# Kernel optimization log

Hardware: AMD Instinct MI355X
Metric: run time of the kernel (lower is better)

## Reference

```python
import jax, jax.numpy as jnp
import numpy as np

D_MODEL = 128; D_STATE = 64; HEADDIM = 64; CHUNK = 64; EXPAND = 2
D_INNER = EXPAND * D_MODEL            # 256
NHEADS = D_INNER // HEADDIM           # 4
NGROUPS = 1; D_CONV = 4
D_XBC = D_INNER + 2 * NGROUPS * D_STATE          # 384
D_IN_PROJ = 2 * D_INNER + 2 * NGROUPS * D_STATE + NHEADS  # 644


def _segsum(x):
    # x: (..., L) -> (..., L, L) with [i, j] = sum_{j<k<=i} x_k, -inf above diag
    L = x.shape[-1]
    cs = jnp.cumsum(x, -1)
    d = cs[..., :, None] - cs[..., None, :]
    mask = jnp.tril(jnp.ones((L, L), bool))
    return jnp.where(mask, d, -jnp.inf)


def _mamba2(x, Wi, conv_w, conv_b, dt_bias, A_log, Dp, norm_w, Wo):
    b, l, _ = x.shape
    zxbcdt = x @ Wi.T                                    # (b,l,644)
    z = zxbcdt[..., :D_INNER]
    xBC = zxbcdt[..., D_INNER:D_INNER + D_XBC]
    dt = jax.nn.softplus(zxbcdt[..., D_INNER + D_XBC:] + dt_bias)  # (b,l,h)
    # causal depthwise conv1d, kernel 4
    xp = jnp.pad(xBC, ((0, 0), (D_CONV - 1, 0), (0, 0)))
    xBC = sum(xp[:, k:k + l, :] * conv_w[:, k] for k in range(D_CONV)) + conv_b
    xBC = jax.nn.silu(xBC)
    xs = xBC[..., :D_INNER].reshape(b, l, NHEADS, HEADDIM)
    Bm = xBC[..., D_INNER:D_INNER + D_STATE]             # (b,l,n) ngroups=1
    Cm = xBC[..., D_INNER + D_STATE:]                    # (b,l,n)
    A = -jnp.exp(A_log)                                  # (h,)
    # chunked SSD (ssd_minimal style)
    c = l // CHUNK
    X = xs.reshape(b, c, CHUNK, NHEADS, HEADDIM)
    dtc = dt.reshape(b, c, CHUNK, NHEADS)
    Bc = Bm.reshape(b, c, CHUNK, D_STATE)
    Cc = Cm.reshape(b, c, CHUNK, D_STATE)
    dA = jnp.transpose(dtc * A, (0, 3, 1, 2))            # (b,h,c,L)
    Acs = jnp.cumsum(dA, -1)
    Lm = jnp.exp(_segsum(dA))                            # (b,h,c,L,L)
    Xdt = X * dtc[..., None]                             # (b,c,L,h,p)
    Yd = jnp.einsum('bcln,bcsn,bhcls,bcshp->bclhp', Cc, Bc, Lm, Xdt)
    dec = jnp.exp(Acs[..., -1:] - Acs)                   # (b,h,c,L)
    st = jnp.einsum('bcln,bhcl,bclhp->bchpn', Bc, dec, Xdt)  # per-chunk states
    cd = jnp.exp(Acs[..., -1])                           # (b,h,c)
    def step(carry, inp):
        s, d = inp                                       # s:(b,h,p,n), d:(b,h)
        return carry * d[..., None, None] + s, carry
    init = jnp.zeros_like(st[:, 0])
    _, prev = jax.lax.scan(step, init, (jnp.moveaxis(st, 1, 0), jnp.moveaxis(cd, 2, 0)))
    prev = jnp.moveaxis(prev, 0, 1)                      # (b,c,h,p,n)
    Yo = jnp.einsum('bcln,bchpn,bhcl->bclhp', Cc, prev, jnp.exp(Acs))
    Y = (Yd + Yo).reshape(b, l, NHEADS, HEADDIM) + Dp[None, None, :, None] * xs
    # gated RMSNorm (norm_before_gate=False)
    y = Y.reshape(b, l, D_INNER) * jax.nn.silu(z)
    y = y * jax.lax.rsqrt(jnp.mean(y * y, -1, keepdims=True) + 1e-5) * norm_w
    return y @ Wo.T


def _init_params(key):
    ks = jax.random.split(key, 5)
    dt = jnp.exp(jax.random.uniform(ks[2], (NHEADS,)) * (np.log(0.1) - np.log(0.001)) + np.log(0.001))
    return {
        'Wi': jax.random.normal(ks[0], (D_IN_PROJ, D_MODEL), jnp.float32) * (D_MODEL ** -0.5),
        'conv_w': jax.random.normal(ks[1], (D_XBC, D_CONV), jnp.float32) * 0.3,
        'conv_b': jnp.zeros((D_XBC,), jnp.float32),
        'dt_bias': jnp.log(jnp.expm1(dt)),
        'A_log': jnp.log(jax.random.uniform(ks[3], (NHEADS,)) * 15.0 + 1.0),
        'D': jnp.ones((NHEADS,), jnp.float32),
        'norm_w': jnp.ones((D_INNER,), jnp.float32),
        'Wo': jax.random.normal(ks[4], (D_MODEL, D_INNER), jnp.float32) * (D_INNER ** -0.5),
    }


def setup_inputs() -> dict:
    key = jax.random.key(0)
    kx, kf, kb = jax.random.split(key, 3)
    inp = {'x': jax.random.normal(kx, (16, 2048, D_MODEL), jnp.float32)}
    for sfx, kk in (('_f', kf), ('_b', kb)):
        p = _init_params(kk)
        for name, v in p.items():
            inp[name + sfx] = v
    return inp


def reference(x, Wi_f, conv_w_f, conv_b_f, dt_bias_f, A_log_f, D_f, norm_w_f, Wo_f,
              Wi_b, conv_w_b, conv_b_b, dt_bias_b, A_log_b, D_b, norm_w_b, Wo_b):
    h_f = _mamba2(x, Wi_f, conv_w_f, conv_b_f, dt_bias_f, A_log_f, D_f, norm_w_f, Wo_f)
    h_b = jnp.flip(_mamba2(jnp.flip(x, 1), Wi_b, conv_w_b, conv_b_b, dt_bias_b, A_log_b, D_b, norm_w_b, Wo_b), 1)
    return h_f + h_b
```

## Files before the change

### kernel.cpp

```cpp
#include <hip/hip_runtime.h>
#include <hip/hip_bf16.h>
#include <cmath>

#define B_    16
#define L_    2048
#define T_    32768
#define DM_   128
#define DI_   256
#define DXBC_ 384
#define DS_   64
#define HD_   64
#define NH_   4
#define NC_   32

typedef __hip_bfloat16 bf16;
typedef __attribute__((ext_vector_type(8))) short short8;
typedef __attribute__((ext_vector_type(4))) float f32x4;

__device__ __forceinline__ float b2f(bf16 v) { return __bfloat162float(v); }
__device__ __forceinline__ bf16  f2b(float f) { return __float2bfloat16(f); }
__device__ __forceinline__ short f2bs(float f) { bf16 h = __float2bfloat16(f); return *reinterpret_cast<short*>(&h); }
__device__ __forceinline__ float bs2f(short s) { bf16 h = *reinterpret_cast<bf16*>(&s); return __bfloat162float(h); }
__device__ __forceinline__ float sigmoidf_(float x) { return 1.f / (1.f + expf(-x)); }
__device__ __forceinline__ float softplusf_(float x) { return (x > 20.f) ? x : log1pf(expf(x)); }
__device__ __forceinline__ float expneg_(float x) { return expf(fminf(x, 0.f)); }

struct __align__(8) S4 { short a, b, c, d; };

#define NWI 82432
#define NWO 32768

__global__ __launch_bounds__(256) void k_prep(
    const float* __restrict__ x,
    const float* __restrict__ WiF, const float* __restrict__ WiB,
    const float* __restrict__ WoF, const float* __restrict__ WoB,
    bf16* __restrict__ Xb, bf16* __restrict__ WiFb, bf16* __restrict__ WiBb,
    bf16* __restrict__ WoFb, bf16* __restrict__ WoBb)
{
    const int gid = blockIdx.x * 256 + threadIdx.x;
    const int stride = gridDim.x * 256;
    for (int i = gid; i < 1048576; i += stride) {
        float4 v = ((const float4*)x)[i];
        S4 s = { f2bs(v.x), f2bs(v.y), f2bs(v.z), f2bs(v.w) };
        ((S4*)Xb)[i] = s;
    }
    for (int i = gid; i < NWI / 4; i += stride) {
        float4 v = ((const float4*)WiF)[i];
        S4 s = { f2bs(v.x), f2bs(v.y), f2bs(v.z), f2bs(v.w) };
        ((S4*)WiFb)[i] = s;
        v = ((const float4*)WiB)[i];
        S4 t = { f2bs(v.x), f2bs(v.y), f2bs(v.z), f2bs(v.w) };
        ((S4*)WiBb)[i] = t;
    }
    for (int i = gid; i < NWO / 4; i += stride) {
        float4 v = ((const float4*)WoF)[i];
        S4 s = { f2bs(v.x), f2bs(v.y), f2bs(v.z), f2bs(v.w) };
        ((S4*)WoFb)[i] = s;
        v = ((const float4*)WoB)[i];
        S4 t = { f2bs(v.x), f2bs(v.y), f2bs(v.z), f2bs(v.w) };
        ((S4*)WoBb)[i] = t;
    }
}

__global__ __launch_bounds__(256) void k_inproj_mfma(
    const bf16* __restrict__ Xb, const bf16* __restrict__ WiFb, const bf16* __restrict__ WiBb,
    const float* __restrict__ cwF, const float* __restrict__ cbF,
    const float* __restrict__ cwB, const float* __restrict__ cbB,
    const float* __restrict__ dtbF, const float* __restrict__ dtbB,
    bf16* __restrict__ Z, bf16* __restrict__ XBC, float* __restrict__ DTV)
{
    const int tid  = threadIdx.x;
    const int wave = tid >> 6, lane = tid & 63;
    const int ln15 = lane & 15, q = lane >> 4;
    const int dir  = blockIdx.y;
    const bf16* Wi = dir ? WiBb : WiFb;
    const int t0 = blockIdx.x * 64;
    const int batch = t0 >> 11, l0 = t0 & (L_ - 1);
    const size_t rowbase = (size_t)dir * T_ + t0;

    __shared__ __align__(16) short xs[80][136];
    __shared__ __align__(16) short smem2[64 * 136];
    short (*ws)[136]  = (short(*)[136])smem2;
    short (*raws)[72] = (short(*)[72])smem2;

    for (int u = tid; u < 1280; u += 256) {
        int r = u >> 4, g = u & 15;
        int l = l0 - 16 + r;
        short8 v = {0, 0, 0, 0, 0, 0, 0, 0};
        if (l >= 0) {
            int sl = dir ? (L_ - 1 - l) : l;
            v = *(const short8*)(Xb + ((size_t)batch * L_ + sl) * DM_ + g * 8);
        }
        *(short8*)&xs[r][g * 8] = v;
    }
    __syncthreads();

    for (int nt = 0; nt <= 10; ++nt) {
        const int c0 = nt * 64;
        __syncthreads();
        if (nt < 10) {
            for (int u = tid; u < 1024; u += 256) {
                int r = u >> 4, g = u & 15;
                *(short8*)&ws[r][g * 8] = *(const short8*)(Wi + (size_t)(c0 + r) * DM_ + g * 8);
            }
        } else {
            for (int u = tid; u < 1024; u += 256) {
                int r = u >> 4, g = u & 15;
                short8 v = {0, 0, 0, 0, 0, 0, 0, 0};
                if (r < 4) v = *(const short8*)(Wi + (size_t)(640 + r) * DM_ + g * 8);
                *(short8*)&ws[r][g * 8] = v;
            }
        }
        __syncthreads();

        f32x4 acc[5];
#pragma unroll
        for (int mt = 0; mt < 5; ++mt) acc[mt] = (f32x4){0.f, 0.f, 0.f, 0.f};
#pragma unroll
        for (int ks = 0; ks < 4; ++ks) {
            short8 bfr = *(const short8*)&ws[16 * wave + ln15][ks * 32 + q * 8];
#pragma unroll
            for (int mt = 0; mt < 5; ++mt) {
                short8 afr = *(const short8*)&xs[16 * mt + ln15][ks * 32 + q * 8];
                acc[mt] = __builtin_amdgcn_mfma_f32_16x16x32_bf16(afr, bfr, acc[mt], 0, 0, 0);
            }
        }

        if (nt == 10) {
            if (wave == 0 && ln15 < 4) {
                const float* dtb = dir ? dtbB : dtbF;
                float bias = dtb[ln15];
#pragma unroll
                for (int mt = 1; mt < 5; ++mt)
#pragma unroll
                    for (int rg = 0; rg < 4; ++rg) {
                        int row = 16 * (mt - 1) + 4 * q + rg;
                        DTV[(rowbase + row) * NH_ + ln15] = softplusf_(acc[mt][rg] + bias);
                    }
            }
            break;
        }

        __syncthreads();
#pragma unroll
        for (int mt = 0; mt < 5; ++mt)
#pragma unroll
            for (int rg = 0; rg < 4; ++rg)
                raws[16 * mt + 4 * q + rg][16 * wave + ln15] = f2bs(acc[mt][rg]);
        __syncthreads();

        if (nt < 4) {
            for (int u = tid; u < 1024; u += 256) {
                int row = u >> 4, c4 = (u & 15) * 4;
                S4 s = *(const S4*)&raws[16 + row][c4];
                *(S4*)(Z + (rowbase + row) * DI_ + c0 + c4) = s;
            }
        } else {
            const float* cw = dir ? cwB : cwF;
            const float* cb = dir ? cbB : cbF;
            for (int u = tid; u < 1024; u += 256) {
                int row = u >> 4, c4 = (u & 15) * 4;
                short o[4];
#pragma unroll
                for (int j = 0; j < 4; ++j) {
                    int ch = c0 - 256 + c4 + j;
                    float s = cb[ch];
#pragma unroll
                    for (int k = 0; k < 4; ++k) s += bs2f(raws[13 + row + k][c4 + j]) * cw[ch * 4 + k];
                    s = s * sigmoidf_(s);
                    o[j] = f2bs(s);
                }
                S4 s4 = { o[0], o[1], o[2], o[3] };
                *(S4*)(XBC + (rowbase + row) * DXBC_ + c0 - 256 + c4) = s4;
            }
        }
    }
}

__global__ __launch_bounds__(256) void k_chunkdiag_mfma(
    const bf16* __restrict__ XBC, const float* __restrict__ DTV,
    const float* __restrict__ AlF, const float* __restrict__ AlB,
    const float* __restrict__ DpF, const float* __restrict__ DpB,
    bf16* __restrict__ Y, bf16* __restrict__ ST, float* __restrict__ CDb)
{
    const int tid = threadIdx.x;
    const int wave = tid >> 6, lane = tid & 63;
    const int ln15 = lane & 15, q = lane >> 4;
    const int c = blockIdx.x;
    const int b = blockIdx.y >> 2;
    const int h = blockIdx.y & 3;
    const int dir = blockIdx.z;
    const float Ah = -expf((dir ? AlB : AlF)[h]);
    const float Dh = (dir ? DpB : DpF)[h];
    const int t0 = b * L_ + c * 64;
    const size_t rowbase = (size_t)dir * T_ + t0;

    __shared__ __align__(16) short Bs[64][72];
    __shared__ __align__(16) short Cs[64][72];
    __shared__ __align__(16) short Xt[64][72];
    __shared__ __align__(16) short Bt[64][72];
    __shared__ float dts[64];
    __shared__ float Acs[64];
    __shared__ float decs[64];

    if (tid < 64) {
        int l = tid;
        float dt = DTV[(rowbase + l) * NH_ + h];
        dts[l] = dt;
        float s = dt * Ah;
#pragma unroll
        for (int off = 1; off < 64; off <<= 1) {
            float t2 = __shfl_up(s, off);
            if (l >= off) s += t2;
        }
        Acs[l] = s;
        float alast = __shfl(s, 63);
        decs[l] = expneg_(alast - s);
        if (l == 0) CDb[(((size_t)dir * B_ + b) * NH_ + h) * NC_ + c] = expneg_(alast);
    }
    __syncthreads();

    for (int u = tid; u < 512; u += 256) {
        int r = u >> 3, g = u & 7;
        size_t base = (rowbase + r) * DXBC_;
        *(short8*)&Bs[r][g * 8] = *(const short8*)(XBC + base + 256 + g * 8);
        *(short8*)&Cs[r][g * 8] = *(const short8*)(XBC + base + 320 + g * 8);
    }
    for (int u = tid; u < 4096; u += 256) {
        int l = u >> 6, p = u & 63;
        Xt[p][l] = f2bs(b2f(XBC[(rowbase + l) * DXBC_ + h * HD_ + p]) * dts[l]);
    }
    for (int u = tid; u < 4096; u += 256) {
        int l = u >> 6, n = u & 63;
        Bt[n][l] = f2bs(b2f(XBC[(rowbase + l) * DXBC_ + 256 + n]) * decs[l]);
    }
    __syncthreads();

    f32x4 a1[4];
#pragma unroll
    for (int ct = 0; ct < 4; ++ct) a1[ct] = (f32x4){0.f, 0.f, 0.f, 0.f};
#pragma unroll
    for (int ks = 0; ks < 2; ++ks) {
        short8 afr = *(const short8*)&Cs[16 * wave + ln15][ks * 32 + q * 8];
#pragma unroll
        for (int ct = 0; ct < 4; ++ct) {
            short8 bfr = *(const short8*)&Bs[16 * ct + ln15][ks * 32 + q * 8];
            a1[ct] = __builtin_amdgcn_mfma_f32_16x16x32_bf16(afr, bfr, a1[ct], 0, 0, 0);
        }
    }
#pragma unroll
    for (int ct = 0; ct < 4; ++ct)
#pragma unroll
        for (int rg = 0; rg < 4; ++rg) {
            int l = 16 * wave + 4 * q + rg, s = 16 * ct + ln15;
            float m = (s <= l) ? a1[ct][rg] * expneg_(Acs[l] - Acs[s]) : 0.f;
            Cs[l][s] = f2bs(m);
        }
    f32x4 a2[4];
#pragma unroll
    for (int ct = 0; ct < 4; ++ct) a2[ct] = (f32x4){0.f, 0.f, 0.f, 0.f};
#pragma unroll
    for (int ks = 0; ks < 2; ++ks) {
        short8 afr = *(const short8*)&Cs[16 * wave + ln15][ks * 32 + q * 8];
#pragma unroll
        for (int ct = 0; ct < 4; ++ct) {
            short8 bfr = *(const short8*)&Xt[16 * ct + ln15][ks * 32 + q * 8];
            a2[ct] = __builtin_amdgcn_mfma_f32_16x16x32_bf16(afr, bfr, a2[ct], 0, 0, 0);
        }
    }
#pragma unroll
    for (int ct = 0; ct < 4; ++ct)
#pragma unroll
        for (int rg = 0; rg < 4; ++rg) {
            int l = 16 * wave + 4 * q + rg, p = 16 * ct + ln15;
            size_t tI = rowbase + l;
            float xraw = b2f(XBC[tI * DXBC_ + h * HD_ + p]);
            Y[tI * DI_ + h * HD_ + p] = f2b(a2[ct][rg] + Dh * xraw);
        }
    f32x4 a3[4];
#pragma unroll
    for (int ct = 0; ct < 4; ++ct) a3[ct] = (f32x4){0.f, 0.f, 0.f, 0.f};
#pragma unroll
    for (int ks = 0; ks < 2; ++ks) {
        short8 afr = *(const short8*)&Xt[16 * wave + ln15][ks * 32 + q * 8];
#pragma unroll
        for (int ct = 0; ct < 4; ++ct) {
            short8 bfr = *(const short8*)&Bt[16 * ct + ln15][ks * 32 + q * 8];
            a3[ct] = __builtin_amdgcn_mfma_f32_16x16x32_bf16(afr, bfr, a3[ct], 0, 0, 0);
        }
    }
    size_t sb = ((((size_t)dir * B_ + b) * NC_ + c) * NH_ + h) * 4096;
#pragma unroll
    for (int ct = 0; ct < 4; ++ct)
#pragma unroll
        for (int rg = 0; rg < 4; ++rg) {
            int p = 16 * wave + 4 * q + rg, n = 16 * ct + ln15;
            ST[sb + p * 64 + n] = f2b(a3[ct][rg]);
        }
}

__global__ __launch_bounds__(256) void k_scan(bf16* __restrict__ ST, const float* __restrict__ CDb)
{
    const int tid = threadIdx.x;
    const int dir = blockIdx.y;
    const int bx = blockIdx.x;
    const int b = bx >> 4, h = (bx >> 2) & 3, qt = bx & 3;
    const size_t cdbase = (((size_t)dir * B_ + b) * NH_ + h) * NC_;
    float carry[4] = {0.f, 0.f, 0.f, 0.f};
    for (int c = 0; c < NC_; ++c) {
        const float cd = CDb[cdbase + c];
        size_t base = ((((size_t)dir * B_ + b) * NC_ + c) * NH_ + h) * 4096 + qt * 1024 + tid;
#pragma unroll
        for (int q = 0; q < 4; ++q) {
            float v = b2f(ST[base + q * 256]);
            ST[base + q * 256] = f2b(carry[q]);
            carry[q] = carry[q] * cd + v;
        }
    }
}

__global__ __launch_bounds__(256) void k_offdiag_fused(
    const bf16* __restrict__ XBC, const float* __restrict__ DTV,
    const float* __restrict__ AlF, const float* __restrict__ AlB,
    const bf16* __restrict__ ST, const bf16* __restrict__ Z,
    const float* __restrict__ nwF, const float* __restrict__ nwB,
    bf16* __restrict__ Y)
{
    const int tid = threadIdx.x;
    const int wave = tid >> 6, lane = tid & 63;
    const int ln15 = lane & 15, q = lane >> 4;
    const int c = blockIdx.x, b = blockIdx.y, dir = blockIdx.z;
    const float* Al = dir ? AlB : AlF;
    const int t0 = b * L_ + c * 64;
    const size_t rowbase = (size_t)dir * T_ + t0;

    __shared__ __align__(16) short Cs[64][72];
    __shared__ __align__(16) short Ps[64][72];
    __shared__ __align__(16) short Yz[64][264];
    __shared__ float eA[NH_][64];

    {
        float A = -expf(Al[wave]);
        float s = DTV[(rowbase + lane) * NH_ + wave] * A;
#pragma unroll
        for (int off = 1; off < 64; off <<= 1) {
            float t2 = __shfl_up(s, off);
            if (lane >= off) s += t2;
        }
        eA[wave][lane] = expneg_(s);
    }
    for (int u = tid; u < 512; u += 256) {
        int r = u >> 3, g = u & 7;
        *(short8*)&Cs[r][g * 8] = *(const short8*)(XBC + (rowbase + r) * DXBC_ + 320 + g * 8);
    }
    for (int u = lane; u < 512; u += 64) {
        int r = 16 * wave + (u >> 5), g = u & 31;
        *(short8*)&Yz[r][g * 8] = *(const short8*)(Y + (rowbase + r) * DI_ + g * 8);
    }

    for (int h = 0; h < NH_; ++h) {
        __syncthreads();
        size_t sb = ((((size_t)dir * B_ + b) * NC_ + c) * NH_ + h) * 4096;
        for (int u = tid; u < 512; u += 256) {
            int r = u >> 3, g = u & 7;
            *(short8*)&Ps[r][g * 8] = *(const short8*)(ST + sb + r * 64 + g * 8);
        }
        __syncthreads();

        f32x4 acc[4];
#pragma unroll
        for (int ct = 0; ct < 4; ++ct) acc[ct] = (f32x4){0.f, 0.f, 0.f, 0.f};
#pragma unroll
        for (int ks = 0; ks < 2; ++ks) {
            short8 afr = *(const short8*)&Cs[16 * wave + ln15][ks * 32 + q * 8];
#pragma unroll
            for (int ct = 0; ct < 4; ++ct) {
                short8 bfr = *(const short8*)&Ps[16 * ct + ln15][ks * 32 + q * 8];
                acc[ct] = __builtin_amdgcn_mfma_f32_16x16x32_bf16(afr, bfr, acc[ct], 0, 0, 0);
            }
        }
#pragma unroll
        for (int ct = 0; ct < 4; ++ct)
#pragma unroll
            for (int rg = 0; rg < 4; ++rg) {
                int l = 16 * wave + 4 * q + rg, p = 16 * ct + ln15;
                float yv = bs2f(Yz[l][h * 64 + p]) + acc[ct][rg] * eA[h][l];
                Yz[l][h * 64 + p] = f2bs(yv);
            }
    }

    const float* nw = dir ? nwB : nwF;
    float nwv[4];
#pragma unroll
    for (int j = 0; j < 4; ++j) nwv[j] = nw[lane * 4 + j];
    for (int rr = 0; rr < 16; ++rr) {
        int row = 16 * wave + rr;
        S4 zv4 = *(const S4*)(Z + (rowbase + row) * DI_ + lane * 4);
        short zr[4] = { zv4.a, zv4.b, zv4.c, zv4.d };
        float v[4]; float ss = 0.f;
#pragma unroll
        for (int j = 0; j < 4; ++j) {
            float yv = bs2f(Yz[row][lane * 4 + j]);
            float zf = bs2f(zr[j]);
            v[j] = yv * zf * sigmoidf_(zf);
            ss += v[j] * v[j];
        }
#pragma unroll
        for (int off = 1; off < 64; off <<= 1) ss += __shfl_xor(ss, off);
        float rn = rsqrtf(ss * (1.f / 256.f) + 1e-5f);
        S4 o = { f2bs(v[0] * rn * nwv[0]), f2bs(v[1] * rn * nwv[1]),
                 f2bs(v[2] * rn * nwv[2]), f2bs(v[3] * rn * nwv[3]) };
        *(S4*)(Y + (rowbase + row) * DI_ + lane * 4) = o;
    }
}

__global__ __launch_bounds__(512) void k_outproj_mfma(
    const bf16* __restrict__ Y, const bf16* __restrict__ WoFb, const bf16* __restrict__ WoBb,
    float* __restrict__ out)
{
    const int tid = threadIdx.x;
    const int wave = tid >> 6, lane = tid & 63;
    const int ln15 = lane & 15, q = lane >> 4;
    const int mt = wave & 3, nh = wave >> 2;
    const int t0 = blockIdx.x * 64;
    const int batch = t0 >> 11;
    const int l0 = t0 & (L_ - 1);

    __shared__ __align__(16) short ys[64][72];
    __shared__ __align__(16) short wsm[128][72];

    f32x4 acc[4];
#pragma unroll
    for (int ct = 0; ct < 4; ++ct) acc[ct] = (f32x4){0.f, 0.f, 0.f, 0.f};

    for (int dir = 0; dir < 2; ++dir) {
        const bf16* Wo = dir ? WoBb : WoFb;
        for (int kt = 0; kt < 4; ++kt) {
            const int k0 = kt * 64;
            __syncthreads();
            {
                int u = tid;
                int r = u >> 3, g = u & 7;
                int tsrc = dir ? (batch * L_ + (L_ - 1 - (l0 + r))) : (t0 + r);
                *(short8*)&ys[r][g * 8] =
                    *(const short8*)(Y + ((size_t)dir * T_ + tsrc) * DI_ + k0 + g * 8);
            }
            for (int u = tid; u < 1024; u += 512) {
                int m = u >> 3, g = u & 7;
                *(short8*)&wsm[m][g * 8] = *(const short8*)(Wo + (size_t)m * DI_ + k0 + g * 8);
            }
            __syncthreads();
#pragma unroll
            for (int ks = 0; ks < 2; ++ks) {
                short8 afr = *(const short8*)&ys[16 * mt + ln15][ks * 32 + q * 8];
#pragma unroll
                for (int ct = 0; ct < 4; ++ct) {
                    short8 bfr = *(const short8*)&wsm[16 * (4 * nh + ct) + ln15][ks * 32 + q * 8];
                    acc[ct] = __builtin_amdgcn_mfma_f32_16x16x32_bf16(afr, bfr, acc[ct], 0, 0, 0);
                }
            }
        }
    }
#pragma unroll
    for (int ct = 0; ct < 4; ++ct)
#pragma unroll
        for (int rg = 0; rg < 4; ++rg) {
            int row = 16 * mt + 4 * q + rg, col = 16 * (4 * nh + ct) + ln15;
            out[((size_t)(t0 + row)) * DM_ + col] = acc[ct][rg];
        }
}

extern "C" void kernel_launch(void* const* d_in, const int* in_sizes, int n_in,
                              void* d_out, int out_size, void* d_ws, size_t ws_size,
                              hipStream_t stream)
{
    const float* x    = (const float*)d_in[0];
    const float* WiF  = (const float*)d_in[1];
    const float* cwF  = (const float*)d_in[2];
    const float* cbF  = (const float*)d_in[3];
    const float* dtbF = (const float*)d_in[4];
    const float* AlF  = (const float*)d_in[5];
    const float* DpF  = (const float*)d_in[6];
    const float* nwF  = (const float*)d_in[7];
    const float* WoF  = (const float*)d_in[8];
    const float* WiB  = (const float*)d_in[9];
    const float* cwB  = (const float*)d_in[10];
    const float* cbB  = (const float*)d_in[11];
    const float* dtbB = (const float*)d_in[12];
    const float* AlB  = (const float*)d_in[13];
    const float* DpB  = (const float*)d_in[14];
    const float* nwB  = (const float*)d_in[15];
    const float* WoB  = (const float*)d_in[16];

    const size_t nZ   = (size_t)2 * T_ * DI_;
    const size_t nXBC = (size_t)2 * T_ * DXBC_;
    const size_t nY   = (size_t)2 * T_ * DI_;
    const size_t nST  = (size_t)2 * B_ * NC_ * NH_ * HD_ * DS_;
    const size_t nWb  = (size_t)2 * NWI + 2 * NWO;
    const size_t nDTV = (size_t)2 * T_ * NH_;
    const size_t nCD  = (size_t)2 * B_ * NH_ * NC_;
    const size_t need = (nZ + nXBC + nY + nST + nWb) * sizeof(bf16)
                      + (nDTV + nCD) * sizeof(float);
    if (ws_size < need) return;

    char* p = (char*)d_ws;
    bf16* Z    = (bf16*)p;            p += nZ * sizeof(bf16);
    bf16* XBC  = (bf16*)p;            p += nXBC * sizeof(bf16);
    bf16* Yb   = (bf16*)p;            p += nY * sizeof(bf16);
    bf16* ST   = (bf16*)p;            p += nST * sizeof(bf16);
    bf16* WiFb = (bf16*)p;            p += (size_t)NWI * sizeof(bf16);
    bf16* WiBb = (bf16*)p;            p += (size_t)NWI * sizeof(bf16);
    bf16* WoFb = (bf16*)p;            p += (size_t)NWO * sizeof(bf16);
    bf16* WoBb = (bf16*)p;            p += (size_t)NWO * sizeof(bf16);
    float* DTV = (float*)p;           p += nDTV * sizeof(float);
    float* CDb = (float*)p;
    bf16* Xb   = ST;

    k_prep<<<2048, 256, 0, stream>>>(x, WiF, WiB, WoF, WoB, Xb, WiFb, WiBb, WoFb, WoBb);
    k_inproj_mfma<<<dim3(512, 2), 256, 0, stream>>>(Xb, WiFb, WiBb, cwF, cbF, cwB, cbB,
                                                    dtbF, dtbB, Z, XBC, DTV);
    k_chunkdiag_mfma<<<dim3(NC_, B_ * NH_, 2), 256, 0, stream>>>(XBC, DTV, AlF, AlB, DpF, DpB,
                                                                 Yb, ST, CDb);
    k_scan<<<dim3(256, 2), 256, 0, stream>>>(ST, CDb);
    k_offdiag_fused<<<dim3(NC_, B_, 2), 256, 0, stream>>>(XBC, DTV, AlF, AlB, ST, Z,
                                                          nwF, nwB, Yb);
    k_outproj_mfma<<<dim3(512), 512, 0, stream>>>(Yb, WoFb, WoBb, (float*)d_out);
}
```

Baseline: 285.6 us.

## Load projection weights directly into registers and restructure in/out projection kernels

The in-projection kernel now reads weight fragments straight from global memory into registers instead of staging them through shared memory. It also splits the Z tiles (written directly from accumulators with swapped MFMA operands), the conv tiles and the dt computation into separate loops, which removes several block barriers. The out-projection kernel drops to 256 threads, stages the full 256-wide Y row once per direction and reads Wo fragments directly from global/L2, so each wave computes all 128 output columns. This is meant to cut LDS traffic and synchronisation, at the cost of more uncoalesced global weight reads and more accumulator registers.

```diff
diff --git a/kernel.cpp b/kernel.cpp
--- a/kernel.cpp
+++ b/kernel.cpp
@@ -79,9 +79,7 @@
     const size_t rowbase = (size_t)dir * T_ + t0;
 
     __shared__ __align__(16) short xs[80][136];
-    __shared__ __align__(16) short smem2[64 * 136];
-    short (*ws)[136]  = (short(*)[136])smem2;
-    short (*raws)[72] = (short(*)[72])smem2;
+    __shared__ __align__(16) short raws[80][80];
 
     for (int u = tid; u < 1280; u += 256) {
         int r = u >> 4, g = u & 15;
@@ -95,52 +93,42 @@
     }
     __syncthreads();
 
-    for (int nt = 0; nt <= 10; ++nt) {
+#pragma unroll
+    for (int zt = 0; zt < 4; ++zt) {
+        const int c0 = zt * 64;
+        short8 wf[4];
+#pragma unroll
+        for (int ks = 0; ks < 4; ++ks)
+            wf[ks] = *(const short8*)(Wi + (size_t)(c0 + 16 * wave + ln15) * DM_ + ks * 32 + q * 8);
+#pragma unroll
+        for (int ct = 0; ct < 4; ++ct) {
+            f32x4 acc = (f32x4){0.f, 0.f, 0.f, 0.f};
+#pragma unroll
+            for (int ks = 0; ks < 4; ++ks) {
+                short8 xf = *(const short8*)&xs[16 + 16 * ct + ln15][ks * 32 + q * 8];
+                acc = __builtin_amdgcn_mfma_f32_16x16x32_bf16(wf[ks], xf, acc, 0, 0, 0);
+            }
+            S4 s = { f2bs(acc[0]), f2bs(acc[1]), f2bs(acc[2]), f2bs(acc[3]) };
+            *(S4*)(Z + (rowbase + 16 * ct + ln15) * DI_ + c0 + 16 * wave + 4 * q) = s;
+        }
+    }
+
+    for (int nt = 4; nt < 10; ++nt) {
         const int c0 = nt * 64;
-        __syncthreads();
-        if (nt < 10) {
-            for (int u = tid; u < 1024; u += 256) {
-                int r = u >> 4, g = u & 15;
-                *(short8*)&ws[r][g * 8] = *(const short8*)(Wi + (size_t)(c0 + r) * DM_ + g * 8);
-            }
-        } else {
-            for (int u = tid; u < 1024; u += 256) {
-                int r = u >> 4, g = u & 15;
-                short8 v = {0, 0, 0, 0, 0, 0, 0, 0};
-                if (r < 4) v = *(const short8*)(Wi + (size_t)(640 + r) * DM_ + g * 8);
-                *(short8*)&ws[r][g * 8] = v;
-            }
-        }
-        __syncthreads();
-
+        short8 bf[4];
+#pragma unroll
+        for (int ks = 0; ks < 4; ++ks)
+            bf[ks] = *(const short8*)(Wi + (size_t)(c0 + 16 * wave + ln15) * DM_ + ks * 32 + q * 8);
         f32x4 acc[5];
 #pragma unroll
         for (int mt = 0; mt < 5; ++mt) acc[mt] = (f32x4){0.f, 0.f, 0.f, 0.f};
 #pragma unroll
-        for (int ks = 0; ks < 4; ++ks) {
-            short8 bfr = *(const short8*)&ws[16 * wave + ln15][ks * 32 + q * 8];
+        for (int ks = 0; ks < 4; ++ks)
 #pragma unroll
             for (int mt = 0; mt < 5; ++mt) {
                 short8 afr = *(const short8*)&xs[16 * mt + ln15][ks * 32 + q * 8];
-                acc[mt] = __builtin_amdgcn_mfma_f32_16x16x32_bf16(afr, bfr, acc[mt], 0, 0, 0);
-            }
-        }
-
-        if (nt == 10) {
-            if (wave == 0 && ln15 < 4) {
-                const float* dtb = dir ? dtbB : dtbF;
-                float bias = dtb[ln15];
-#pragma unroll
-                for (int mt = 1; mt < 5; ++mt)
-#pragma unroll
-                    for (int rg = 0; rg < 4; ++rg) {
-                        int row = 16 * (mt - 1) + 4 * q + rg;
-                        DTV[(rowbase + row) * NH_ + ln15] = softplusf_(acc[mt][rg] + bias);
-                    }
-            }
-            break;
-        }
-
+                acc[mt] = __builtin_amdgcn_mfma_f32_16x16x32_bf16(afr, bf[ks], acc[mt], 0, 0, 0);
+            }
         __syncthreads();
 #pragma unroll
         for (int mt = 0; mt < 5; ++mt)
@@ -149,29 +137,51 @@
                 raws[16 * mt + 4 * q + rg][16 * wave + ln15] = f2bs(acc[mt][rg]);
         __syncthreads();
 
-        if (nt < 4) {
-            for (int u = tid; u < 1024; u += 256) {
-                int row = u >> 4, c4 = (u & 15) * 4;
-                S4 s = *(const S4*)&raws[16 + row][c4];
-                *(S4*)(Z + (rowbase + row) * DI_ + c0 + c4) = s;
-            }
-        } else {
-            const float* cw = dir ? cwB : cwF;
-            const float* cb = dir ? cbB : cbF;
-            for (int u = tid; u < 1024; u += 256) {
-                int row = u >> 4, c4 = (u & 15) * 4;
-                short o[4];
-#pragma unroll
-                for (int j = 0; j < 4; ++j) {
-                    int ch = c0 - 256 + c4 + j;
-                    float s = cb[ch];
-#pragma unroll
-                    for (int k = 0; k < 4; ++k) s += bs2f(raws[13 + row + k][c4 + j]) * cw[ch * 4 + k];
-                    s = s * sigmoidf_(s);
-                    o[j] = f2bs(s);
-                }
-                S4 s4 = { o[0], o[1], o[2], o[3] };
-                *(S4*)(XBC + (rowbase + row) * DXBC_ + c0 - 256 + c4) = s4;
+        const float* cw = dir ? cwB : cwF;
+        const float* cb = dir ? cbB : cbF;
+        for (int u = tid; u < 1024; u += 256) {
+            int row = u >> 4, c4 = (u & 15) * 4;
+            float s0[4];
+            int ch0 = c0 - 256 + c4;
+#pragma unroll
+            for (int j = 0; j < 4; ++j) s0[j] = cb[ch0 + j];
+#pragma unroll
+            for (int k = 0; k < 4; ++k) {
+                S4 rv = *(const S4*)&raws[13 + row + k][c4];
+                short rr[4] = { rv.a, rv.b, rv.c, rv.d };
+#pragma unroll
+                for (int j = 0; j < 4; ++j) s0[j] += bs2f(rr[j]) * cw[(ch0 + j) * 4 + k];
+            }
+            short o[4];
+#pragma unroll
+            for (int j = 0; j < 4; ++j) { float s = s0[j]; s = s * sigmoidf_(s); o[j] = f2bs(s); }
+            S4 s4 = { o[0], o[1], o[2], o[3] };
+            *(S4*)(XBC + (rowbase + row) * DXBC_ + ch0) = s4;
+        }
+    }
+
+    if (wave == 0) {
+        short8 bf[4];
+#pragma unroll
+        for (int ks = 0; ks < 4; ++ks) {
+            short8 v = {0, 0, 0, 0, 0, 0, 0, 0};
+            if (ln15 < 4) v = *(const short8*)(Wi + (size_t)(640 + ln15) * DM_ + ks * 32 + q * 8);
+            bf[ks] = v;
+        }
+        const float* dtb = dir ? dtbB : dtbF;
+#pragma unroll
+        for (int s = 0; s < 4; ++s) {
+            f32x4 acc = (f32x4){0.f, 0.f, 0.f, 0.f};
+#pragma unroll
+            for (int ks = 0; ks < 4; ++ks) {
+                short8 afr = *(const short8*)&xs[16 + 16 * s + ln15][ks * 32 + q * 8];
+                acc = __builtin_amdgcn_mfma_f32_16x16x32_bf16(afr, bf[ks], acc, 0, 0, 0);
+            }
+            if (ln15 < 4) {
+                float bias = dtb[ln15];
+#pragma unroll
+                for (int rg = 0; rg < 4; ++rg)
+                    DTV[(rowbase + 16 * s + 4 * q + rg) * NH_ + ln15] = softplusf_(acc[rg] + bias);
             }
         }
     }
@@ -414,58 +424,48 @@
     }
 }
 
-__global__ __launch_bounds__(512) void k_outproj_mfma(
+__global__ __launch_bounds__(256) void k_outproj_mfma(
     const bf16* __restrict__ Y, const bf16* __restrict__ WoFb, const bf16* __restrict__ WoBb,
     float* __restrict__ out)
 {
     const int tid = threadIdx.x;
     const int wave = tid >> 6, lane = tid & 63;
     const int ln15 = lane & 15, q = lane >> 4;
-    const int mt = wave & 3, nh = wave >> 2;
     const int t0 = blockIdx.x * 64;
     const int batch = t0 >> 11;
     const int l0 = t0 & (L_ - 1);
 
-    __shared__ __align__(16) short ys[64][72];
-    __shared__ __align__(16) short wsm[128][72];
-
-    f32x4 acc[4];
-#pragma unroll
-    for (int ct = 0; ct < 4; ++ct) acc[ct] = (f32x4){0.f, 0.f, 0.f, 0.f};
+    __shared__ __align__(16) short ys[64][264];
+
+    f32x4 acc[8];
+#pragma unroll
+    for (int ct = 0; ct < 8; ++ct) acc[ct] = (f32x4){0.f, 0.f, 0.f, 0.f};
 
     for (int dir = 0; dir < 2; ++dir) {
         const bf16* Wo = dir ? WoBb : WoFb;
-        for (int kt = 0; kt < 4; ++kt) {
-            const int k0 = kt * 64;
-            __syncthreads();
-            {
-                int u = tid;
-                int r = u >> 3, g = u & 7;
-                int tsrc = dir ? (batch * L_ + (L_ - 1 - (l0 + r))) : (t0 + r);
-                *(short8*)&ys[r][g * 8] =
-                    *(const short8*)(Y + ((size_t)dir * T_ + tsrc) * DI_ + k0 + g * 8);
-            }
-            for (int u = tid; u < 1024; u += 512) {
-                int m = u >> 3, g = u & 7;
-                *(short8*)&wsm[m][g * 8] = *(const short8*)(Wo + (size_t)m * DI_ + k0 + g * 8);
-            }
-            __syncthreads();
-#pragma unroll
-            for (int ks = 0; ks < 2; ++ks) {
-                short8 afr = *(const short8*)&ys[16 * mt + ln15][ks * 32 + q * 8];
-#pragma unroll
-                for (int ct = 0; ct < 4; ++ct) {
-                    short8 bfr = *(const short8*)&wsm[16 * (4 * nh + ct) + ln15][ks * 32 + q * 8];
-                    acc[ct] = __builtin_amdgcn_mfma_f32_16x16x32_bf16(afr, bfr, acc[ct], 0, 0, 0);
-                }
-            }
-        }
-    }
-#pragma unroll
-    for (int ct = 0; ct < 4; ++ct)
+        __syncthreads();
+        for (int u = tid; u < 2048; u += 256) {
+            int r = u >> 5, g = u & 31;
+            int tsrc = dir ? (batch * L_ + (L_ - 1 - (l0 + r))) : (t0 + r);
+            *(short8*)&ys[r][g * 8] =
+                *(const short8*)(Y + ((size_t)dir * T_ + tsrc) * DI_ + g * 8);
+        }
+        __syncthreads();
+#pragma unroll
+        for (int kk = 0; kk < 8; ++kk) {
+            short8 afr = *(const short8*)&ys[16 * wave + ln15][kk * 32 + q * 8];
+#pragma unroll
+            for (int ct = 0; ct < 8; ++ct) {
+                short8 bfr = *(const short8*)(Wo + (size_t)(16 * ct + ln15) * DI_ + kk * 32 + q * 8);
+                acc[ct] = __builtin_amdgcn_mfma_f32_16x16x32_bf16(afr, bfr, acc[ct], 0, 0, 0);
+            }
+        }
+    }
+#pragma unroll
+    for (int ct = 0; ct < 8; ++ct)
 #pragma unroll
         for (int rg = 0; rg < 4; ++rg) {
-            int row = 16 * mt + 4 * q + rg, col = 16 * (4 * nh + ct) + ln15;
+            int row = 16 * wave + 4 * q + rg, col = 16 * ct + ln15;
             out[((size_t)(t0 + row)) * DM_ + col] = acc[ct][rg];
         }
 }
@@ -524,5 +524,5 @@
     k_scan<<<dim3(256, 2), 256, 0, stream>>>(ST, CDb);
     k_offdiag_fused<<<dim3(NC_, B_, 2), 256, 0, stream>>>(XBC, DTV, AlF, AlB, ST, Z,
                                                           nwF, nwB, Yb);
-    k_outproj_mfma<<<dim3(512), 512, 0, stream>>>(Yb, WoFb, WoBb, (float*)d_out);
-}
+    k_outproj_mfma<<<dim3(512), 256, 0, stream>>>(Yb, WoFb, WoBb, (float*)d_out);
+}
```

Result: no change. 289.2 us (+1.2%).
